# Optimization experiments

Hardware: AMD Instinct MI355X
Metric: run time of the kernel (lower is better)

## Reference

```python
import jax, jax.numpy as jnp
import numpy as np
from functools import partial

L, B, D_IN, D_MODEL, D_OUT, D_STATE = 2048, 8, 128, 256, 32, 16
D_INNER, DT_RANK, K_CONV = 2 * D_MODEL, D_MODEL // 16, 4
LOG2PI = float(np.log(2.0 * np.pi))


def setup_inputs() -> dict:
    key = jax.random.key(0)
    ks = jax.random.split(key, 16)
    sc = 0.02
    inp = {
        "s": jax.random.normal(ks[0], (L, B, D_IN), jnp.float32),
        "a": jax.random.normal(ks[1], (L, B, D_OUT), jnp.float32),
        # embedding linear
        "W_emb": jax.random.normal(ks[2], (D_IN, D_MODEL), jnp.float32) * sc,
        "b_emb": jnp.zeros((D_MODEL,), jnp.float32),
        # mamba block params
        "norm_w": jnp.ones((D_MODEL,), jnp.float32),
        "W_in": jax.random.normal(ks[3], (D_MODEL, 2 * D_INNER), jnp.float32) * sc,
        "conv_w": jax.random.normal(ks[4], (D_INNER, 1, K_CONV), jnp.float32) * sc,
        "conv_b": jnp.zeros((D_INNER,), jnp.float32),
        "W_x": jax.random.normal(ks[5], (D_INNER, DT_RANK + 2 * D_STATE), jnp.float32) * sc,
        "W_dt": jax.random.normal(ks[6], (DT_RANK, D_INNER), jnp.float32) * sc,
        "b_dt": jnp.full((D_INNER,), -2.0, jnp.float32),  # softplus(-2) ~ small init dt
        "A_log": jnp.broadcast_to(jnp.log(jnp.arange(1, D_STATE + 1, dtype=jnp.float32)), (D_INNER, D_STATE)).copy(),
        "D": jnp.ones((D_INNER,), jnp.float32),
        "W_out": jax.random.normal(ks[7], (D_INNER, D_MODEL), jnp.float32) * sc,
        # action head + log_std
        "W_head": jax.random.normal(ks[8], (D_MODEL, D_OUT), jnp.float32) * sc,
        "b_head": jnp.zeros((D_OUT,), jnp.float32),
        "log_std": jnp.zeros((D_OUT,), jnp.float32),
    }
    return inp


def _rmsnorm(x, w, eps=1e-5):
    return x * jax.lax.rsqrt(jnp.mean(x * x, axis=-1, keepdims=True) + eps) * w


def _silu(x):
    return x * jax.nn.sigmoid(x)


def _mamba_block(x, norm_w, W_in, conv_w, conv_b, W_x, W_dt, b_dt, A_log, D, W_out):
    # x: (B, L, d_model)
    resid = x
    xn = _rmsnorm(x, norm_w)
    xz = xn @ W_in                                  # (B, L, 2*d_inner)
    xp, z = jnp.split(xz, 2, axis=-1)
    # causal depthwise conv over time
    xc = jax.lax.conv_general_dilated(
        xp.transpose(0, 2, 1), conv_w, window_strides=(1,),
        padding=[(K_CONV - 1, 0)], feature_group_count=D_INNER,
        dimension_numbers=("NCH", "OIH", "NCH"))
    xp = _silu((xc + conv_b[None, :, None]).transpose(0, 2, 1))  # (B, L, d_inner)
    # input-dependent SSM params
    x_dbl = xp @ W_x                                # (B, L, dt_rank + 2*d_state)
    dt, Bm, Cm = jnp.split(x_dbl, [DT_RANK, DT_RANK + D_STATE], axis=-1)
    dt = jax.nn.softplus(dt @ W_dt + b_dt)          # (B, L, d_inner)
    A = -jnp.exp(A_log)                             # (d_inner, d_state)

    def step(h, t):
        dt_t, B_t, C_t, x_t = t                     # (B,d_i) (B,d_s) (B,d_s) (B,d_i)
        dA = jnp.exp(dt_t[..., None] * A)           # (B, d_inner, d_state)
        dBx = (dt_t * x_t)[..., None] * B_t[:, None, :]
        h = dA * h + dBx
        y = jnp.einsum("bds,bs->bd", h, C_t)
        return h, y

    h0 = jnp.zeros((x.shape[0], D_INNER, D_STATE), x.dtype)
    tm = lambda u: jnp.moveaxis(u, 1, 0)            # time-major
    _, ys = jax.lax.scan(step, h0, (tm(dt), tm(Bm), tm(Cm), tm(xp)))
    y = jnp.moveaxis(ys, 0, 1) + xp * D             # (B, L, d_inner)
    y = y * _silu(z)
    return y @ W_out + resid


def reference(s, a, W_emb, b_emb, norm_w, W_in, conv_w, conv_b, W_x, W_dt, b_dt,
              A_log, D, W_out, W_head, b_head, log_std):
    x = s @ W_emb + b_emb                           # (L, B, d_model)
    x = x.transpose(1, 0, 2)                        # (B, L, d_model)
    x = _mamba_block(x, norm_w, W_in, conv_w, conv_b, W_x, W_dt, b_dt, A_log, D, W_out)
    x = x.transpose(1, 0, 2)                        # (L, B, d_model)
    mu = x @ W_head + b_head                        # (L, B, d_out)
    # Normal(mu, exp(log_std)).log_prob(a).sum(-1)
    z = (a - mu) * jnp.exp(-log_std)
    logp = -0.5 * z * z - log_std - 0.5 * LOG2PI
    return logp.sum(axis=-1)                        # (L, B)
```

## Files before the change

### kernel.cpp

```cpp
#include <hip/hip_runtime.h>

typedef unsigned short u16;
typedef short bf16x8 __attribute__((ext_vector_type(8)));
typedef float floatx4 __attribute__((ext_vector_type(4)));

#define LSEQ 2048
#define BB 8
#define NTOK (LSEQ*BB)
#define DMODEL 256
#define DINNER 512
#define NSEG 128
#define SEG_N 32
#define SEG_L 64

__device__ __forceinline__ float siluf(float x){ return x / (1.f + __expf(-x)); }
__device__ __forceinline__ float b2f(u16 x){ return __uint_as_float(((unsigned)x) << 16); }
__device__ __forceinline__ u16 f2b(float f){
  unsigned u = __float_as_uint(f);
  unsigned r = (u + 0x7fffu + ((u >> 16) & 1u)) >> 16;
  return (u16)r;
}

__device__ __forceinline__ void gload16(const u16* g, u16* l) {
  __builtin_amdgcn_global_load_lds(
      (const __attribute__((address_space(1))) unsigned int*)g,
      (__attribute__((address_space(3))) unsigned int*)l, 16, 0, 0);
}

__device__ __forceinline__ void compute_dA(float dt, float As0, bool uni,
    const float* __restrict__ Alog, int c, float* dA)
{
  if (uni) {
    float p = __expf(dt*As0);
    float p2 = p*p, p4 = p2*p2, p8 = p4*p4;
    dA[0]=p;      dA[1]=p2;     dA[2]=p2*p;   dA[3]=p4;
    dA[4]=p4*p;   dA[5]=p4*p2;  dA[6]=p4*p2*p;dA[7]=p8;
    dA[8]=p8*p;   dA[9]=p8*p2;  dA[10]=p8*p2*p; dA[11]=p8*p4;
    dA[12]=p8*p4*p; dA[13]=p8*p4*p2; dA[14]=p8*p4*p2*p; dA[15]=p8*p8;
  } else {
    #pragma unroll
    for (int s = 0; s < 16; ++s) dA[s] = __expf(dt * (-__expf(Alog[c*16+s])));
  }
}

__global__ __launch_bounds__(256) void prep_k(
    const float* __restrict__ Wemb, const float* __restrict__ Win,
    const float* __restrict__ Wout, const float* __restrict__ Wx,
    const float* __restrict__ Wh,
    u16* __restrict__ WTe, u16* __restrict__ WTi, u16* __restrict__ WTo,
    u16* __restrict__ WxT, u16* __restrict__ WhT)
{
  __shared__ u16 T[64*66];
  int g = blockIdx.x, tid = threadIdx.x;
  if (g < 96) {
    const float* src; u16* dst; int n0, k0, srcld, dstld;
    if (g < 64) {
      int tn = g & 15, tk = g >> 4;
      n0 = tn*64; k0 = tk*64; src = Win; dst = WTi; srcld = 1024; dstld = 256;
    } else {
      int g2 = g - 64;
      int tn = g2 & 3, tk = g2 >> 2;
      n0 = tn*64; k0 = tk*64; src = Wout; dst = WTo; srcld = 256; dstld = 512;
    }
    int rr = tid >> 6, cc = tid & 63;
    #pragma unroll
    for (int p = 0; p < 16; ++p) {
      int kr = p*4 + rr;
      T[kr*66 + cc] = f2b(src[(size_t)(k0+kr)*srcld + n0 + cc]);
    }
    __syncthreads();
    #pragma unroll
    for (int p = 0; p < 16; ++p) {
      int nr = p*4 + rr;
      dst[(size_t)(n0+nr)*dstld + k0 + cc] = T[cc*66 + nr];
    }
  } else if (g < 224) {
    int idx = (g-96)*256 + tid; int n = idx >> 7, k = idx & 127;
    WTe[idx] = f2b(Wemb[(size_t)k*256 + n]);
  } else if (g < 320) {
    int idx = (g-224)*256 + tid; int n = idx >> 9, k = idx & 511;
    WxT[idx] = f2b(Wx[(size_t)k*48 + n]);
  } else {
    int idx = (g-320)*256 + tid; int j = idx >> 8, k = idx & 255;
    WhT[idx] = f2b(Wh[(size_t)k*32 + j]);
  }
}

__global__ __launch_bounds__(256) void embnorm_k(
    const float* __restrict__ s, const u16* __restrict__ WTe,
    const float* __restrict__ bemb, const float* __restrict__ nw,
    u16* __restrict__ Xb, u16* __restrict__ XNb)
{
  __shared__ u16 SH[64*264];
  __shared__ float ssq[64*4];
  __shared__ float rr[64];
  u16* As = SH;
  u16* Bs = SH + 64*40;
  const int tid = threadIdx.x;
  const int wave = tid >> 6, lane = tid & 63;
  const int quad = lane >> 4, l16 = lane & 15;
  const int m0 = blockIdx.x*64;
  const int wn = wave*64;
  const int srow = tid >> 2, sch = (tid & 3)*8;
  floatx4 acc[4][4];
  #pragma unroll
  for (int r = 0; r < 4; ++r)
    #pragma unroll
    for (int c = 0; c < 4; ++c) acc[r][c] = (floatx4){0.f,0.f,0.f,0.f};

  for (int k0 = 0; k0 < 128; k0 += 32) {
    {
      float4 v0 = *(const float4*)&s[(size_t)(m0+srow)*128 + k0 + sch];
      float4 v1 = *(const float4*)&s[(size_t)(m0+srow)*128 + k0 + sch + 4];
      __align__(16) u16 o[8];
      o[0]=f2b(v0.x); o[1]=f2b(v0.y); o[2]=f2b(v0.z); o[3]=f2b(v0.w);
      o[4]=f2b(v1.x); o[5]=f2b(v1.y); o[6]=f2b(v1.z); o[7]=f2b(v1.w);
      *(uint4*)&As[srow*40 + sch] = *(const uint4*)o;
    }
    #pragma unroll
    for (int p = 0; p < 4; ++p) {
      int row = srow + p*64;
      *(uint4*)&Bs[row*40 + sch] = *(const uint4*)&WTe[(size_t)row*128 + k0 + sch];
    }
    __syncthreads();
    bf16x8 af[4], bf[4];
    #pragma unroll
    for (int r = 0; r < 4; ++r) af[r] = *(const bf16x8*)&As[(r*16 + l16)*40 + quad*8];
    #pragma unroll
    for (int c = 0; c < 4; ++c) bf[c] = *(const bf16x8*)&Bs[(wn + c*16 + l16)*40 + quad*8];
    #pragma unroll
    for (int r = 0; r < 4; ++r)
      #pragma unroll
      for (int c = 0; c < 4; ++c)
        acc[r][c] = __builtin_amdgcn_mfma_f32_16x16x32_bf16(af[r], bf[c], acc[r][c], 0, 0, 0);
    __syncthreads();
  }
  u16* Xs = SH;
  #pragma unroll
  for (int c = 0; c < 4; ++c) {
    int n = wn + c*16 + l16;
    float bv = bemb[n];
    #pragma unroll
    for (int r = 0; r < 4; ++r)
      #pragma unroll
      for (int reg = 0; reg < 4; ++reg) {
        int ml = r*16 + quad*4 + reg;
        Xs[ml*264 + n] = f2b(acc[r][c][reg] + bv);
      }
  }
  __syncthreads();
  #pragma unroll
  for (int p = 0; p < 8; ++p) {
    int row = p*8 + (tid >> 5);
    int col = (tid & 31)*8;
    *(uint4*)&Xb[(size_t)(m0+row)*256 + col] = *(const uint4*)&Xs[row*264 + col];
  }
  const int tk = tid >> 2, q = tid & 3;
  float ss = 0.f;
  #pragma unroll
  for (int j = 0; j < 8; ++j) {
    uint4 v = *(const uint4*)&Xs[tk*264 + q*64 + j*8];
    const u16* u = (const u16*)&v;
    #pragma unroll
    for (int i = 0; i < 8; ++i) { float x = b2f(u[i]); ss += x*x; }
  }
  ssq[tk*4 + q] = ss;
  __syncthreads();
  if (q == 0)
    rr[tk] = rsqrtf((ssq[tk*4]+ssq[tk*4+1]+ssq[tk*4+2]+ssq[tk*4+3])*(1.f/DMODEL) + 1e-5f);
  __syncthreads();
  float r = rr[tk];
  #pragma unroll
  for (int j = 0; j < 8; ++j) {
    int idx = q*64 + j*8;
    uint4 v = *(const uint4*)&Xs[tk*264 + idx];
    const u16* u = (const u16*)&v;
    float4 w0 = *(const float4*)&nw[idx];
    float4 w1 = *(const float4*)&nw[idx+4];
    __align__(16) u16 o[8];
    o[0]=f2b(b2f(u[0])*r*w0.x); o[1]=f2b(b2f(u[1])*r*w0.y);
    o[2]=f2b(b2f(u[2])*r*w0.z); o[3]=f2b(b2f(u[3])*r*w0.w);
    o[4]=f2b(b2f(u[4])*r*w1.x); o[5]=f2b(b2f(u[5])*r*w1.y);
    o[6]=f2b(b2f(u[6])*r*w1.z); o[7]=f2b(b2f(u[7])*r*w1.w);
    *(uint4*)&XNb[(size_t)(m0+tk)*256 + idx] = *(const uint4*)o;
  }
}

template<int K>
__global__ __launch_bounds__(256) void gemm_mfma(
    const u16* __restrict__ Ab, const u16* __restrict__ WT,
    u16* __restrict__ Cv, int N)
{
  __shared__ __align__(16) u16 SH[17408];
  u16* As = SH;
  u16* Bs = SH + 128*64;
  const int tid = threadIdx.x;
  const int wave = tid >> 6, lane = tid & 63;
  const int quad = lane >> 4, l16 = lane & 15;
  const int bm0 = blockIdx.x*128, bn0 = blockIdx.y*128;
  const int wm = (wave & 1)*64, wn = (wave >> 1)*64;
  floatx4 acc[4][4];
  #pragma unroll
  for (int r = 0; r < 4; ++r)
    #pragma unroll
    for (int c = 0; c < 4; ++c) acc[r][c] = (floatx4){0.f,0.f,0.f,0.f};

  for (int k0 = 0; k0 < K; k0 += 64) {
    #pragma unroll
    for (int p = 0; p < 4; ++p) {
      int cid = (wave*4 + p)*64 + lane;
      int row = cid >> 3, sch = (cid & 7) ^ (row & 7);
      gload16(&Ab[(size_t)(bm0+row)*K + k0 + sch*8], As + (wave*4+p)*512);
      gload16(&WT[(size_t)(bn0+row)*K + k0 + sch*8], Bs + (wave*4+p)*512);
    }
    __syncthreads();
    #pragma unroll
    for (int ks = 0; ks < 2; ++ks) {
      bf16x8 af[4], bf[4];
      #pragma unroll
      for (int r = 0; r < 4; ++r) {
        int row = wm + r*16 + l16;
        int lch = (ks*4 + quad) ^ (row & 7);
        af[r] = *(const bf16x8*)&As[row*64 + lch*8];
      }
      #pragma unroll
      for (int c = 0; c < 4; ++c) {
        int row = wn + c*16 + l16;
        int lch = (ks*4 + quad) ^ (row & 7);
        bf[c] = *(const bf16x8*)&Bs[row*64 + lch*8];
      }
      #pragma unroll
      for (int r = 0; r < 4; ++r)
        #pragma unroll
        for (int c = 0; c < 4; ++c)
          acc[r][c] = __builtin_amdgcn_mfma_f32_16x16x32_bf16(af[r], bf[c], acc[r][c], 0, 0, 0);
    }
    __syncthreads();
  }
  u16* Cs = SH;
  #pragma unroll
  for (int c = 0; c < 4; ++c) {
    int nl = wn + c*16 + l16;
    #pragma unroll
    for (int r = 0; r < 4; ++r)
      #pragma unroll
      for (int reg = 0; reg < 4; ++reg) {
        int ml = wm + r*16 + quad*4 + reg;
        Cs[ml*136 + nl] = f2b(acc[r][c][reg]);
      }
  }
  __syncthreads();
  #pragma unroll
  for (int p = 0; p < 8; ++p) {
    int row = p*16 + (tid >> 4);
    int col = (tid & 15)*8;
    uint4 v = *(const uint4*)&Cs[row*136 + col];
    *(uint4*)&Cv[(size_t)(bm0+row)*N + bn0 + col] = v;
  }
}

__global__ __launch_bounds__(256) void xdblBC_k(const u16* __restrict__ XZb,
    const float* __restrict__ cw, const float* __restrict__ cb,
    const u16* __restrict__ WxT,
    float* __restrict__ BM, float* __restrict__ CM, float* __restrict__ DTR,
    u16* __restrict__ XPb)
{
  __shared__ u16 As[64*40];
  __shared__ u16 Ws[48*40];
  __shared__ float CWs[512*4];
  __shared__ float CBs[512];
  const int tid = threadIdx.x;
  const int wave = tid >> 6, lane = tid & 63;
  const int quad = lane >> 4, l16 = lane & 15;
  const int m0 = blockIdx.x*64;
  const int srow = tid >> 2, sch = (tid & 3)*8;
  const int n = m0 + srow;
  for (int e = tid; e < 2048; e += 256) CWs[e] = cw[e];
  for (int e = tid; e < 512;  e += 256) CBs[e] = cb[e];
  floatx4 acc[3];
  #pragma unroll
  for (int j = 0; j < 3; ++j) acc[j] = (floatx4){0.f,0.f,0.f,0.f};
  __syncthreads();
  const bf16x8 z8 = {0,0,0,0,0,0,0,0};
  for (int k0 = 0; k0 < DINNER; k0 += 32) {
    bf16x8 t3 = *(const bf16x8*)&XZb[(size_t)n*1024 + k0 + sch];
    bf16x8 t2 = z8, t1 = z8, t0v = z8;
    if (n >= 8)  t2  = *(const bf16x8*)&XZb[(size_t)(n-8)*1024  + k0 + sch];
    if (n >= 16) t1  = *(const bf16x8*)&XZb[(size_t)(n-16)*1024 + k0 + sch];
    if (n >= 24) t0v = *(const bf16x8*)&XZb[(size_t)(n-24)*1024 + k0 + sch];
    __align__(16) u16 outa[8];
    #pragma unroll
    for (int j = 0; j < 8; ++j) {
      int c = k0 + sch + j;
      float4 wv = *(const float4*)&CWs[c*4];
      float xc = CBs[c] + wv.x*b2f((u16)t0v[j]) + wv.y*b2f((u16)t1[j])
               + wv.z*b2f((u16)t2[j]) + wv.w*b2f((u16)t3[j]);
      outa[j] = f2b(siluf(xc));
    }
    *(uint4*)&As[srow*40 + sch] = *(const uint4*)outa;
    *(uint4*)&XPb[(size_t)n*DINNER + k0 + sch] = *(const uint4*)outa;
    if (tid < 192) {
      int wr = tid >> 2;
      *(uint4*)&Ws[wr*40 + sch] = *(const uint4*)&WxT[(size_t)wr*512 + k0 + sch];
    }
    __syncthreads();
    bf16x8 af = *(const bf16x8*)&As[(wave*16 + l16)*40 + quad*8];
    #pragma unroll
    for (int j = 0; j < 3; ++j) {
      bf16x8 bf = *(const bf16x8*)&Ws[(j*16 + l16)*40 + quad*8];
      acc[j] = __builtin_amdgcn_mfma_f32_16x16x32_bf16(af, bf, acc[j], 0, 0, 0);
    }
    __syncthreads();
  }
  const int tok0 = m0 + wave*16;
  #pragma unroll
  for (int reg = 0; reg < 4; ++reg) {
    size_t t = (size_t)(tok0 + quad*4 + reg);
    BM[t*16 + l16]  = acc[1][reg];
    CM[t*16 + l16]  = acc[2][reg];
    DTR[t*16 + l16] = acc[0][reg];
  }
}

__global__ __launch_bounds__(256) void scanA_k(const float* __restrict__ DTR,
    const u16* __restrict__ XPb, const float* __restrict__ BM,
    const float* __restrict__ Wdt, const float* __restrict__ bdt,
    const float* __restrict__ Alog, u16* __restrict__ HENDb,
    float* __restrict__ DTS, unsigned* __restrict__ DXb)
{
  __shared__ float ROWa[SEG_L*16];
  __shared__ float ROWb[SEG_L*16];
  const int tid = threadIdx.x;
  const int seg = blockIdx.x, b = blockIdx.y, half = blockIdx.z;
  const int c = half*256 + tid;
  const int t0 = seg*SEG_L;
  const size_t base = (size_t)t0*BB + b;
  for (int idx = tid; idx < SEG_L*16; idx += 256) {
    int t = idx >> 4, j = idx & 15;
    size_t off = (base + (size_t)t*BB)*16 + j;
    ROWa[idx] = BM[off];
    ROWb[idx] = DTR[off];
  }
  float As0 = -__expf(Alog[c*16]);
  bool uni = true;
  #pragma unroll
  for (int s = 1; s < 16; ++s) {
    float Av = -__expf(Alog[c*16+s]);
    uni = uni && (fabsf(Av - As0*(float)(s+1)) <= 1e-4f*(float)(s+1));
  }
  float wdt[16];
  #pragma unroll
  for (int r = 0; r < 16; ++r) wdt[r] = Wdt[r*DINNER + c];
  const float bd = bdt[c];
  float h[16];
  #pragma unroll
  for (int s = 0; s < 16; ++s) h[s] = 0.f;
  float dts = 0.f;
  const u16* xpp = XPb + base*DINNER + c;
  __syncthreads();
  float xp = b2f(xpp[0]);
  for (int t = 0; t < SEG_L; ++t) {
    float xpn = (t+1 < SEG_L) ? b2f(xpp[(size_t)(t+1)*BB*DINNER]) : 0.f;
    float dsum = bd;
    #pragma unroll
    for (int r = 0; r < 16; ++r) dsum = fmaf(ROWb[t*16+r], wdt[r], dsum);
    float dt = (dsum > 20.f) ? dsum : __logf(1.f + __expf(dsum));
    dts += dt;
    DXb[(((size_t)(t0+t)*BB + b)*DINNER + c)] = ((unsigned)f2b(xp) << 16) | f2b(dt);
    float dtx = dt * xp;
    float dA[16];
    compute_dA(dt, As0, uni, Alog, c, dA);
    float4 r0 = *(const float4*)&ROWa[t*16 + 0];
    float4 r1 = *(const float4*)&ROWa[t*16 + 4];
    float4 r2 = *(const float4*)&ROWa[t*16 + 8];
    float4 r3 = *(const float4*)&ROWa[t*16 + 12];
    h[0]  = fmaf(dA[0],  h[0],  dtx*r0.x);
    h[1]  = fmaf(dA[1],  h[1],  dtx*r0.y);
    h[2]  = fmaf(dA[2],  h[2],  dtx*r0.z);
    h[3]  = fmaf(dA[3],  h[3],  dtx*r0.w);
    h[4]  = fmaf(dA[4],  h[4],  dtx*r1.x);
    h[5]  = fmaf(dA[5],  h[5],  dtx*r1.y);
    h[6]  = fmaf(dA[6],  h[6],  dtx*r1.z);
    h[7]  = fmaf(dA[7],  h[7],  dtx*r1.w);
    h[8]  = fmaf(dA[8],  h[8],  dtx*r2.x);
    h[9]  = fmaf(dA[9],  h[9],  dtx*r2.y);
    h[10] = fmaf(dA[10], h[10], dtx*r2.z);
    h[11] = fmaf(dA[11], h[11], dtx*r2.w);
    h[12] = fmaf(dA[12], h[12], dtx*r3.x);
    h[13] = fmaf(dA[13], h[13], dtx*r3.y);
    h[14] = fmaf(dA[14], h[14], dtx*r3.z);
    h[15] = fmaf(dA[15], h[15], dtx*r3.w);
    xp = xpn;
  }
  u16* hp = &HENDb[(((size_t)seg*BB + b)*DINNER + c)*16];
  #pragma unroll
  for (int q = 0; q < 2; ++q) {
    ushort4 v0, v1;
    v0.x = f2b(h[q*8+0]); v0.y = f2b(h[q*8+1]); v0.z = f2b(h[q*8+2]); v0.w = f2b(h[q*8+3]);
    v1.x = f2b(h[q*8+4]); v1.y = f2b(h[q*8+5]); v1.z = f2b(h[q*8+6]); v1.w = f2b(h[q*8+7]);
    *(ushort4*)&hp[q*8]     = v0;
    *(ushort4*)&hp[q*8 + 4] = v1;
  }
  DTS[((size_t)seg*BB + b)*DINNER + c] = dts;
}

__global__ __launch_bounds__(256) void scanC_k(const unsigned* __restrict__ DXb,
    const u16* __restrict__ XZb, const float* __restrict__ BM, const float* __restrict__ CM,
    const float* __restrict__ Alog, const float* __restrict__ Dp,
    const u16* __restrict__ HENDb, const float* __restrict__ DTS,
    u16* __restrict__ YGb)
{
  __shared__ float ROWa[SEG_L*16];
  __shared__ float ROWc[SEG_L*16];
  const int tid = threadIdx.x;
  const int seg = (SEG_N - 1) - blockIdx.x;
  const int b = blockIdx.y, half = blockIdx.z;
  const int c = half*256 + tid;
  const int t0 = seg*SEG_L;
  const size_t base = (size_t)t0*BB + b;
  for (int idx = tid; idx < SEG_L*16; idx += 256) {
    int t = idx >> 4, j = idx & 15;
    size_t off = (base + (size_t)t*BB)*16 + j;
    ROWa[idx] = BM[off];
    ROWc[idx] = CM[off];
  }
  float As0 = -__expf(Alog[c*16]);
  bool uni = true;
  #pragma unroll
  for (int s = 1; s < 16; ++s) {
    float Av = -__expf(Alog[c*16+s]);
    uni = uni && (fabsf(Av - As0*(float)(s+1)) <= 1e-4f*(float)(s+1));
  }
  float h[16];
  #pragma unroll
  for (int s = 0; s < 16; ++s) h[s] = 0.f;
  if (seg > 0) {
    float ds = DTS[((size_t)0*BB + b)*DINNER + c];
    const u16* hp0 = &HENDb[(((size_t)0*BB + b)*DINNER + c)*16];
    ushort4 a0 = *(const ushort4*)&hp0[0];
    ushort4 a1 = *(const ushort4*)&hp0[4];
    ushort4 a2 = *(const ushort4*)&hp0[8];
    ushort4 a3 = *(const ushort4*)&hp0[12];
    for (int k = 0; k < seg; ++k) {
      float dsn = 0.f;
      ushort4 n0, n1, n2, n3;
      if (k+1 < seg) {
        dsn = DTS[((size_t)(k+1)*BB + b)*DINNER + c];
        const u16* hpn = &HENDb[(((size_t)(k+1)*BB + b)*DINNER + c)*16];
        n0 = *(const ushort4*)&hpn[0];
        n1 = *(const ushort4*)&hpn[4];
        n2 = *(const ushort4*)&hpn[8];
        n3 = *(const ushort4*)&hpn[12];
      }
      float dA[16];
      compute_dA(ds, As0, uni, Alog, c, dA);
      h[0]  = fmaf(h[0],  dA[0],  b2f(a0.x));
      h[1]  = fmaf(h[1],  dA[1],  b2f(a0.y));
      h[2]  = fmaf(h[2],  dA[2],  b2f(a0.z));
      h[3]  = fmaf(h[3],  dA[3],  b2f(a0.w));
      h[4]  = fmaf(h[4],  dA[4],  b2f(a1.x));
      h[5]  = fmaf(h[5],  dA[5],  b2f(a1.y));
      h[6]  = fmaf(h[6],  dA[6],  b2f(a1.z));
      h[7]  = fmaf(h[7],  dA[7],  b2f(a1.w));
      h[8]  = fmaf(h[8],  dA[8],  b2f(a2.x));
      h[9]  = fmaf(h[9],  dA[9],  b2f(a2.y));
      h[10] = fmaf(h[10], dA[10], b2f(a2.z));
      h[11] = fmaf(h[11], dA[11], b2f(a2.w));
      h[12] = fmaf(h[12], dA[12], b2f(a3.x));
      h[13] = fmaf(h[13], dA[13], b2f(a3.y));
      h[14] = fmaf(h[14], dA[14], b2f(a3.z));
      h[15] = fmaf(h[15], dA[15], b2f(a3.w));
      ds = dsn; a0 = n0; a1 = n1; a2 = n2; a3 = n3;
    }
  }
  const float Dv = Dp[c];
  const unsigned* dxp = DXb + base*DINNER + c;
  const u16* zp  = XZb + base*1024 + DINNER + c;
  u16*       ygp = YGb + base*DINNER + c;
  __syncthreads();
  unsigned dx = dxp[0];
  float zg = b2f(zp[0]);
  for (int t = 0; t < SEG_L; ++t) {
    unsigned dxn = 0; float zgn = 0.f;
    if (t+1 < SEG_L) {
      dxn = dxp[(size_t)(t+1)*BB*DINNER];
      zgn = b2f(zp[(size_t)(t+1)*BB*1024]);
    }
    float dt = __uint_as_float(dx << 16);
    float xp = __uint_as_float(dx & 0xffff0000u);
    float dtx = dt * xp;
    float dA[16];
    compute_dA(dt, As0, uni, Alog, c, dA);
    float4 ra0 = *(const float4*)&ROWa[t*16 + 0];
    float4 ra1 = *(const float4*)&ROWa[t*16 + 4];
    float4 ra2 = *(const float4*)&ROWa[t*16 + 8];
    float4 ra3 = *(const float4*)&ROWa[t*16 + 12];
    float4 rc0 = *(const float4*)&ROWc[t*16 + 0];
    float4 rc1 = *(const float4*)&ROWc[t*16 + 4];
    float4 rc2 = *(const float4*)&ROWc[t*16 + 8];
    float4 rc3 = *(const float4*)&ROWc[t*16 + 12];
    float y0 = 0.f, y1 = 0.f, y2 = 0.f, y3 = 0.f;
    h[0]  = fmaf(dA[0],  h[0],  dtx*ra0.x); y0 = fmaf(h[0],  rc0.x, y0);
    h[1]  = fmaf(dA[1],  h[1],  dtx*ra0.y); y1 = fmaf(h[1],  rc0.y, y1);
    h[2]  = fmaf(dA[2],  h[2],  dtx*ra0.z); y2 = fmaf(h[2],  rc0.z, y2);
    h[3]  = fmaf(dA[3],  h[3],  dtx*ra0.w); y3 = fmaf(h[3],  rc0.w, y3);
    h[4]  = fmaf(dA[4],  h[4],  dtx*ra1.x); y0 = fmaf(h[4],  rc1.x, y0);
    h[5]  = fmaf(dA[5],  h[5],  dtx*ra1.y); y1 = fmaf(h[5],  rc1.y, y1);
    h[6]  = fmaf(dA[6],  h[6],  dtx*ra1.z); y2 = fmaf(h[6],  rc1.z, y2);
    h[7]  = fmaf(dA[7],  h[7],  dtx*ra1.w); y3 = fmaf(h[7],  rc1.w, y3);
    h[8]  = fmaf(dA[8],  h[8],  dtx*ra2.x); y0 = fmaf(h[8],  rc2.x, y0);
    h[9]  = fmaf(dA[9],  h[9],  dtx*ra2.y); y1 = fmaf(h[9],  rc2.y, y1);
    h[10] = fmaf(dA[10], h[10], dtx*ra2.z); y2 = fmaf(h[10], rc2.z, y2);
    h[11] = fmaf(dA[11], h[11], dtx*ra2.w); y3 = fmaf(h[11], rc2.w, y3);
    h[12] = fmaf(dA[12], h[12], dtx*ra3.x); y0 = fmaf(h[12], rc3.x, y0);
    h[13] = fmaf(dA[13], h[13], dtx*ra3.y); y1 = fmaf(h[13], rc3.y, y1);
    h[14] = fmaf(dA[14], h[14], dtx*ra3.z); y2 = fmaf(h[14], rc3.z, y2);
    h[15] = fmaf(dA[15], h[15], dtx*ra3.w); y3 = fmaf(h[15], rc3.w, y3);
    float y = (y0+y1) + (y2+y3);
    ygp[(size_t)t*BB*DINNER] = f2b((y + xp*Dv) * siluf(zg));
    dx = dxn; zg = zgn;
  }
}

__global__ __launch_bounds__(256) void outhead_k(const u16* __restrict__ YGb,
    const u16* __restrict__ WTo, const u16* __restrict__ Xb,
    const u16* __restrict__ WhT, const float* __restrict__ bh,
    const float* __restrict__ lstd, const float* __restrict__ a,
    float* __restrict__ out)
{
  __shared__ u16 SH[(64+256)*72];
  u16* As = SH;
  u16* Bs = SH + 64*72;
  const int tid = threadIdx.x;
  const int wave = tid >> 6, lane = tid & 63;
  const int quad = lane >> 4, l16 = lane & 15;
  const int m0 = blockIdx.x*64;
  const int n0 = wave*64;
  const int srow = tid >> 3, sch = (tid & 7)*8;
  floatx4 acc[4][4];
  #pragma unroll
  for (int r = 0; r < 4; ++r)
    #pragma unroll
    for (int c = 0; c < 4; ++c) acc[r][c] = (floatx4){0.f,0.f,0.f,0.f};

  for (int k0 = 0; k0 < DINNER; k0 += 64) {
    #pragma unroll
    for (int p = 0; p < 2; ++p) {
      int row = srow + p*32;
      *(uint4*)&As[row*72 + sch] = *(const uint4*)&YGb[(size_t)(m0+row)*DINNER + k0 + sch];
    }
    #pragma unroll
    for (int p = 0; p < 8; ++p) {
      int row = srow + p*32;
      *(uint4*)&Bs[row*72 + sch] = *(const uint4*)&WTo[(size_t)row*DINNER + k0 + sch];
    }
    __syncthreads();
    #pragma unroll
    for (int ks = 0; ks < 2; ++ks) {
      bf16x8 af[4], bf[4];
      #pragma unroll
      for (int r = 0; r < 4; ++r)
        af[r] = *(const bf16x8*)&As[(r*16 + l16)*72 + ks*32 + quad*8];
      #pragma unroll
      for (int c = 0; c < 4; ++c)
        bf[c] = *(const bf16x8*)&Bs[(n0 + c*16 + l16)*72 + ks*32 + quad*8];
      #pragma unroll
      for (int r = 0; r < 4; ++r)
        #pragma unroll
        for (int c = 0; c < 4; ++c)
          acc[r][c] = __builtin_amdgcn_mfma_f32_16x16x32_bf16(af[r], bf[c], acc[r][c], 0, 0, 0);
    }
    __syncthreads();
  }
  u16* Xs = SH;
  #pragma unroll
  for (int p = 0; p < 8; ++p) {
    int row = p*8 + (tid >> 5);
    int col = (tid & 31)*8;
    *(uint4*)&Xs[row*264 + col] = *(const uint4*)&Xb[(size_t)(m0+row)*256 + col];
  }
  __syncthreads();
  #pragma unroll
  for (int c = 0; c < 4; ++c) {
    int n = n0 + c*16 + l16;
    #pragma unroll
    for (int r = 0; r < 4; ++r) {
      #pragma unroll
      for (int reg = 0; reg < 4; ++reg) {
        int ml = r*16 + quad*4 + reg;
        Xs[ml*264 + n] = f2b(acc[r][c][reg] + b2f(Xs[ml*264 + n]));
      }
    }
  }
  __syncthreads();
  floatx4 mu[2];
  mu[0] = (floatx4){0.f,0.f,0.f,0.f};
  mu[1] = (floatx4){0.f,0.f,0.f,0.f};
  #pragma unroll
  for (int k0 = 0; k0 < DMODEL; k0 += 32) {
    bf16x8 axf = *(const bf16x8*)&Xs[(wave*16 + l16)*264 + k0 + quad*8];
    #pragma unroll
    for (int nt = 0; nt < 2; ++nt) {
      bf16x8 bwf = *(const bf16x8*)(WhT + (size_t)(nt*16 + l16)*DMODEL + k0 + quad*8);
      mu[nt] = __builtin_amdgcn_mfma_f32_16x16x32_bf16(axf, bwf, mu[nt], 0, 0, 0);
    }
  }
  float ls0 = lstd[l16],      els0 = __expf(-ls0), bh0 = bh[l16];
  float ls1 = lstd[16 + l16], els1 = __expf(-ls1), bh1 = bh[16 + l16];
  #pragma unroll
  for (int reg = 0; reg < 4; ++reg) {
    int tok = m0 + wave*16 + quad*4 + reg;
    float m0v = mu[0][reg] + bh0;
    float m1v = mu[1][reg] + bh1;
    float z0 = (a[(size_t)tok*32 + l16]      - m0v) * els0;
    float z1 = (a[(size_t)tok*32 + 16 + l16] - m1v) * els1;
    float t = (-0.5f*z0*z0 - ls0) + (-0.5f*z1*z1 - ls1) - 2.f*0.91893853320467274f;
    t += __shfl_xor(t, 1);
    t += __shfl_xor(t, 2);
    t += __shfl_xor(t, 4);
    t += __shfl_xor(t, 8);
    if (l16 == 0) out[tok] = t;
  }
}

extern "C" void kernel_launch(void* const* d_in, const int* in_sizes, int n_in,
                              void* d_out, int out_size, void* d_ws, size_t ws_size,
                              hipStream_t stream)
{
  const float* s    = (const float*)d_in[0];
  const float* a    = (const float*)d_in[1];
  const float* Wemb = (const float*)d_in[2];
  const float* bemb = (const float*)d_in[3];
  const float* nw   = (const float*)d_in[4];
  const float* Win  = (const float*)d_in[5];
  const float* cw   = (const float*)d_in[6];
  const float* cb   = (const float*)d_in[7];
  const float* Wx   = (const float*)d_in[8];
  const float* Wdt  = (const float*)d_in[9];
  const float* bdt  = (const float*)d_in[10];
  const float* Alog = (const float*)d_in[11];
  const float* Dp   = (const float*)d_in[12];
  const float* Wout = (const float*)d_in[13];
  const float* Wh   = (const float*)d_in[14];
  const float* bh   = (const float*)d_in[15];
  const float* lstd = (const float*)d_in[16];

  u16*   Xb   = (u16*)d_ws;
  u16*   XZb  = Xb  + (size_t)NTOK*DMODEL;
  u16*   XNb  = XZb + (size_t)NTOK*1024;
  u16*   YGb  = XNb + (size_t)NTOK*DMODEL;
  u16*   WTe  = YGb + (size_t)NTOK*DINNER;
  u16*   WTi  = WTe + 256*128;
  u16*   WTo  = WTi + 1024*256;
  u16*   WxT  = WTo + 256*512;
  u16*   WhT  = WxT + 48*512;
  u16*   HENDb= WhT + 32*256;
  u16*   XPb  = HENDb + (size_t)NSEG*BB*DINNER*16;
  unsigned* DXb = (unsigned*)(XPb + (size_t)NTOK*DINNER);
  float* BM   = (float*)(DXb + (size_t)NTOK*DINNER);
  float* CM   = BM + (size_t)NTOK*16;
  float* DTR  = CM + (size_t)NTOK*16;
  float* DTS  = DTR + (size_t)NTOK*16;
  float* out  = (float*)d_out;

  prep_k        <<<352,         256, 0, stream>>>(Wemb, Win, Wout, Wx, Wh,
                                                  WTe, WTi, WTo, WxT, WhT);
  embnorm_k     <<<256,         256, 0, stream>>>(s, WTe, bemb, nw, Xb, XNb);
  gemm_mfma<256><<<dim3(128,8), 256, 0, stream>>>(XNb, WTi, XZb, 1024);
  xdblBC_k      <<<256,         256, 0, stream>>>(XZb, cw, cb, WxT, BM, CM, DTR, XPb);
  scanA_k       <<<dim3(SEG_N,BB,2), 256, 0, stream>>>(DTR, XPb, BM, Wdt, bdt,
                                                       Alog, HENDb, DTS, DXb);
  scanC_k       <<<dim3(SEG_N,BB,2), 256, 0, stream>>>(DXb, XZb, BM, CM,
                                                       Alog, Dp, HENDb, DTS, YGb);
  outhead_k     <<<256,         256, 0, stream>>>(YGb, WTo, Xb, WhT, bh, lstd, a, out);
}
```

Baseline: 241.2 us.

## Split scan state across lane pairs and halve segment length

Each channel's 16-element SSM state is now split across two half-waves of 8 states each. Partial dt and y sums are combined with a cross-lane shuffle, and the segment count doubles to 64 segments of length 32. Both scan kernels launch four times as many threads with fewer registers each, which raises parallelism and shortens the sequential time loop. In exchange there are extra shuffles, duplicated dt computation, half-idle lanes on stores, and a longer serial cross-segment combine in scanC.

After: 269.3 us. +11.7%, slower.

```diff
diff --git a/kernel.cpp b/kernel.cpp
--- a/kernel.cpp
+++ b/kernel.cpp
@@ -10,8 +10,8 @@
 #define DMODEL 256
 #define DINNER 512
 #define NSEG 128
-#define SEG_N 32
-#define SEG_L 64
+#define SEG_N 64
+#define SEG_L 32
 
 __device__ __forceinline__ float siluf(float x){ return x / (1.f + __expf(-x)); }
 __device__ __forceinline__ float b2f(u16 x){ return __uint_as_float(((unsigned)x) << 16); }
@@ -27,19 +27,19 @@
       (__attribute__((address_space(3))) unsigned int*)l, 16, 0, 0);
 }
 
-__device__ __forceinline__ void compute_dA(float dt, float As0, bool uni,
-    const float* __restrict__ Alog, int c, float* dA)
+__device__ __forceinline__ void compute_dA8(float dt, float As0, bool uni,
+    const float* __restrict__ Alog, int c, int so, float* dA)
 {
   if (uni) {
     float p = __expf(dt*As0);
-    float p2 = p*p, p4 = p2*p2, p8 = p4*p4;
-    dA[0]=p;      dA[1]=p2;     dA[2]=p2*p;   dA[3]=p4;
-    dA[4]=p4*p;   dA[5]=p4*p2;  dA[6]=p4*p2*p;dA[7]=p8;
-    dA[8]=p8*p;   dA[9]=p8*p2;  dA[10]=p8*p2*p; dA[11]=p8*p4;
-    dA[12]=p8*p4*p; dA[13]=p8*p4*p2; dA[14]=p8*p4*p2*p; dA[15]=p8*p8;
+    float p2 = p*p, p3 = p2*p, p4 = p2*p2;
+    float p5 = p4*p, p6 = p4*p2, p7 = p4*p3, p8 = p4*p4;
+    float f = so ? p8 : 1.f;
+    dA[0]=p*f;  dA[1]=p2*f; dA[2]=p3*f; dA[3]=p4*f;
+    dA[4]=p5*f; dA[5]=p6*f; dA[6]=p7*f; dA[7]=p8*f;
   } else {
     #pragma unroll
-    for (int s = 0; s < 16; ++s) dA[s] = __expf(dt * (-__expf(Alog[c*16+s])));
+    for (int j = 0; j < 8; ++j) dA[j] = __expf(dt * (-__expf(Alog[c*16+so+j])));
   }
 }
 
@@ -331,8 +331,10 @@
   __shared__ float ROWa[SEG_L*16];
   __shared__ float ROWb[SEG_L*16];
   const int tid = threadIdx.x;
-  const int seg = blockIdx.x, b = blockIdx.y, half = blockIdx.z;
-  const int c = half*256 + tid;
+  const int wave = tid >> 6, lane = tid & 63;
+  const int sgrp = lane >> 5, so = sgrp*8;
+  const int seg = blockIdx.x, b = blockIdx.y;
+  const int c = blockIdx.z*128 + wave*32 + (lane & 31);
   const int t0 = seg*SEG_L;
   const size_t base = (size_t)t0*BB + b;
   for (int idx = tid; idx < SEG_L*16; idx += 256) {
@@ -348,60 +350,51 @@
     float Av = -__expf(Alog[c*16+s]);
     uni = uni && (fabsf(Av - As0*(float)(s+1)) <= 1e-4f*(float)(s+1));
   }
-  float wdt[16];
-  #pragma unroll
-  for (int r = 0; r < 16; ++r) wdt[r] = Wdt[r*DINNER + c];
+  float wdt[8];
+  #pragma unroll
+  for (int r = 0; r < 8; ++r) wdt[r] = Wdt[(so + r)*DINNER + c];
   const float bd = bdt[c];
-  float h[16];
-  #pragma unroll
-  for (int s = 0; s < 16; ++s) h[s] = 0.f;
+  float h[8];
+  #pragma unroll
+  for (int j = 0; j < 8; ++j) h[j] = 0.f;
   float dts = 0.f;
   const u16* xpp = XPb + base*DINNER + c;
   __syncthreads();
   float xp = b2f(xpp[0]);
   for (int t = 0; t < SEG_L; ++t) {
     float xpn = (t+1 < SEG_L) ? b2f(xpp[(size_t)(t+1)*BB*DINNER]) : 0.f;
-    float dsum = bd;
-    #pragma unroll
-    for (int r = 0; r < 16; ++r) dsum = fmaf(ROWb[t*16+r], wdt[r], dsum);
+    float dpart = sgrp ? 0.f : bd;
+    #pragma unroll
+    for (int r = 0; r < 8; ++r) dpart = fmaf(ROWb[t*16 + so + r], wdt[r], dpart);
+    float dsum = dpart + __shfl_xor(dpart, 32);
     float dt = (dsum > 20.f) ? dsum : __logf(1.f + __expf(dsum));
     dts += dt;
-    DXb[(((size_t)(t0+t)*BB + b)*DINNER + c)] = ((unsigned)f2b(xp) << 16) | f2b(dt);
+    if (sgrp == 0)
+      DXb[(((size_t)(t0+t)*BB + b)*DINNER + c)] = ((unsigned)f2b(xp) << 16) | f2b(dt);
     float dtx = dt * xp;
-    float dA[16];
-    compute_dA(dt, As0, uni, Alog, c, dA);
-    float4 r0 = *(const float4*)&ROWa[t*16 + 0];
-    float4 r1 = *(const float4*)&ROWa[t*16 + 4];
-    float4 r2 = *(const float4*)&ROWa[t*16 + 8];
-    float4 r3 = *(const float4*)&ROWa[t*16 + 12];
-    h[0]  = fmaf(dA[0],  h[0],  dtx*r0.x);
-    h[1]  = fmaf(dA[1],  h[1],  dtx*r0.y);
-    h[2]  = fmaf(dA[2],  h[2],  dtx*r0.z);
-    h[3]  = fmaf(dA[3],  h[3],  dtx*r0.w);
-    h[4]  = fmaf(dA[4],  h[4],  dtx*r1.x);
-    h[5]  = fmaf(dA[5],  h[5],  dtx*r1.y);
-    h[6]  = fmaf(dA[6],  h[6],  dtx*r1.z);
-    h[7]  = fmaf(dA[7],  h[7],  dtx*r1.w);
-    h[8]  = fmaf(dA[8],  h[8],  dtx*r2.x);
-    h[9]  = fmaf(dA[9],  h[9],  dtx*r2.y);
-    h[10] = fmaf(dA[10], h[10], dtx*r2.z);
-    h[11] = fmaf(dA[11], h[11], dtx*r2.w);
-    h[12] = fmaf(dA[12], h[12], dtx*r3.x);
-    h[13] = fmaf(dA[13], h[13], dtx*r3.y);
-    h[14] = fmaf(dA[14], h[14], dtx*r3.z);
-    h[15] = fmaf(dA[15], h[15], dtx*r3.w);
+    float dA[8];
+    compute_dA8(dt, As0, uni, Alog, c, so, dA);
+    float4 r0 = *(const float4*)&ROWa[t*16 + so + 0];
+    float4 r1 = *(const float4*)&ROWa[t*16 + so + 4];
+    h[0] = fmaf(dA[0], h[0], dtx*r0.x);
+    h[1] = fmaf(dA[1], h[1], dtx*r0.y);
+    h[2] = fmaf(dA[2], h[2], dtx*r0.z);
+    h[3] = fmaf(dA[3], h[3], dtx*r0.w);
+    h[4] = fmaf(dA[4], h[4], dtx*r1.x);
+    h[5] = fmaf(dA[5], h[5], dtx*r1.y);
+    h[6] = fmaf(dA[6], h[6], dtx*r1.z);
+    h[7] = fmaf(dA[7], h[7], dtx*r1.w);
     xp = xpn;
   }
-  u16* hp = &HENDb[(((size_t)seg*BB + b)*DINNER + c)*16];
-  #pragma unroll
-  for (int q = 0; q < 2; ++q) {
-    ushort4 v0, v1;
-    v0.x = f2b(h[q*8+0]); v0.y = f2b(h[q*8+1]); v0.z = f2b(h[q*8+2]); v0.w = f2b(h[q*8+3]);
-    v1.x = f2b(h[q*8+4]); v1.y = f2b(h[q*8+5]); v1.z = f2b(h[q*8+6]); v1.w = f2b(h[q*8+7]);
-    *(ushort4*)&hp[q*8]     = v0;
-    *(ushort4*)&hp[q*8 + 4] = v1;
-  }
-  DTS[((size_t)seg*BB + b)*DINNER + c] = dts;
+  {
+    __align__(16) u16 o[8];
+    #pragma unroll
+    for (int j = 0; j < 8; ++j) o[j] = f2b(h[j]);
+    u16* hp = &HENDb[(((size_t)seg*BB + b)*DINNER + c)*16 + so];
+    *(uint4*)hp = *(const uint4*)o;
+  }
+  if (sgrp == 0)
+    DTS[((size_t)seg*BB + b)*DINNER + c] = dts;
 }
 
 __global__ __launch_bounds__(256) void scanC_k(const unsigned* __restrict__ DXb,
@@ -413,9 +406,11 @@
   __shared__ float ROWa[SEG_L*16];
   __shared__ float ROWc[SEG_L*16];
   const int tid = threadIdx.x;
+  const int wave = tid >> 6, lane = tid & 63;
+  const int sgrp = lane >> 5, so = sgrp*8;
   const int seg = (SEG_N - 1) - blockIdx.x;
-  const int b = blockIdx.y, half = blockIdx.z;
-  const int c = half*256 + tid;
+  const int b = blockIdx.y;
+  const int c = blockIdx.z*128 + wave*32 + (lane & 31);
   const int t0 = seg*SEG_L;
   const size_t base = (size_t)t0*BB + b;
   for (int idx = tid; idx < SEG_L*16; idx += 256) {
@@ -431,46 +426,31 @@
     float Av = -__expf(Alog[c*16+s]);
     uni = uni && (fabsf(Av - As0*(float)(s+1)) <= 1e-4f*(float)(s+1));
   }
-  float h[16];
-  #pragma unroll
-  for (int s = 0; s < 16; ++s) h[s] = 0.f;
+  float h[8];
+  #pragma unroll
+  for (int j = 0; j < 8; ++j) h[j] = 0.f;
   if (seg > 0) {
     float ds = DTS[((size_t)0*BB + b)*DINNER + c];
-    const u16* hp0 = &HENDb[(((size_t)0*BB + b)*DINNER + c)*16];
-    ushort4 a0 = *(const ushort4*)&hp0[0];
-    ushort4 a1 = *(const ushort4*)&hp0[4];
-    ushort4 a2 = *(const ushort4*)&hp0[8];
-    ushort4 a3 = *(const ushort4*)&hp0[12];
+    uint4 hv = *(const uint4*)&HENDb[(((size_t)0*BB + b)*DINNER + c)*16 + so];
     for (int k = 0; k < seg; ++k) {
       float dsn = 0.f;
-      ushort4 n0, n1, n2, n3;
+      uint4 hn = hv;
       if (k+1 < seg) {
         dsn = DTS[((size_t)(k+1)*BB + b)*DINNER + c];
-        const u16* hpn = &HENDb[(((size_t)(k+1)*BB + b)*DINNER + c)*16];
-        n0 = *(const ushort4*)&hpn[0];
-        n1 = *(const ushort4*)&hpn[4];
-        n2 = *(const ushort4*)&hpn[8];
-        n3 = *(const ushort4*)&hpn[12];
+        hn = *(const uint4*)&HENDb[(((size_t)(k+1)*BB + b)*DINNER + c)*16 + so];
       }
-      float dA[16];
-      compute_dA(ds, As0, uni, Alog, c, dA);
-      h[0]  = fmaf(h[0],  dA[0],  b2f(a0.x));
-      h[1]  = fmaf(h[1],  dA[1],  b2f(a0.y));
-      h[2]  = fmaf(h[2],  dA[2],  b2f(a0.z));
-      h[3]  = fmaf(h[3],  dA[3],  b2f(a0.w));
-      h[4]  = fmaf(h[4],  dA[4],  b2f(a1.x));
-      h[5]  = fmaf(h[5],  dA[5],  b2f(a1.y));
-      h[6]  = fmaf(h[6],  dA[6],  b2f(a1.z));
-      h[7]  = fmaf(h[7],  dA[7],  b2f(a1.w));
-      h[8]  = fmaf(h[8],  dA[8],  b2f(a2.x));
-      h[9]  = fmaf(h[9],  dA[9],  b2f(a2.y));
-      h[10] = fmaf(h[10], dA[10], b2f(a2.z));
-      h[11] = fmaf(h[11], dA[11], b2f(a2.w));
-      h[12] = fmaf(h[12], dA[12], b2f(a3.x));
-      h[13] = fmaf(h[13], dA[13], b2f(a3.y));
-      h[14] = fmaf(h[14], dA[14], b2f(a3.z));
-      h[15] = fmaf(h[15], dA[15], b2f(a3.w));
-      ds = dsn; a0 = n0; a1 = n1; a2 = n2; a3 = n3;
+      const u16* he = (const u16*)&hv;
+      float dA[8];
+      compute_dA8(ds, As0, uni, Alog, c, so, dA);
+      h[0] = fmaf(h[0], dA[0], b2f(he[0]));
+      h[1] = fmaf(h[1], dA[1], b2f(he[1]));
+      h[2] = fmaf(h[2], dA[2], b2f(he[2]));
+      h[3] = fmaf(h[3], dA[3], b2f(he[3]));
+      h[4] = fmaf(h[4], dA[4], b2f(he[4]));
+      h[5] = fmaf(h[5], dA[5], b2f(he[5]));
+      h[6] = fmaf(h[6], dA[6], b2f(he[6]));
+      h[7] = fmaf(h[7], dA[7], b2f(he[7]));
+      ds = dsn; hv = hn;
     }
   }
   const float Dv = Dp[c];
@@ -489,35 +469,25 @@
     float dt = __uint_as_float(dx << 16);
     float xp = __uint_as_float(dx & 0xffff0000u);
     float dtx = dt * xp;
-    float dA[16];
-    compute_dA(dt, As0, uni, Alog, c, dA);
-    float4 ra0 = *(const float4*)&ROWa[t*16 + 0];
-    float4 ra1 = *(const float4*)&ROWa[t*16 + 4];
-    float4 ra2 = *(const float4*)&ROWa[t*16 + 8];
-    float4 ra3 = *(const float4*)&ROWa[t*16 + 12];
-    float4 rc0 = *(const float4*)&ROWc[t*16 + 0];
-    float4 rc1 = *(const float4*)&ROWc[t*16 + 4];
-    float4 rc2 = *(const float4*)&ROWc[t*16 + 8];
-    float4 rc3 = *(const float4*)&ROWc[t*16 + 12];
+    float dA[8];
+    compute_dA8(dt, As0, uni, Alog, c, so, dA);
+    float4 ra0 = *(const float4*)&ROWa[t*16 + so + 0];
+    float4 ra1 = *(const float4*)&ROWa[t*16 + so + 4];
+    float4 rc0 = *(const float4*)&ROWc[t*16 + so + 0];
+    float4 rc1 = *(const float4*)&ROWc[t*16 + so + 4];
     float y0 = 0.f, y1 = 0.f, y2 = 0.f, y3 = 0.f;
-    h[0]  = fmaf(dA[0],  h[0],  dtx*ra0.x); y0 = fmaf(h[0],  rc0.x, y0);
-    h[1]  = fmaf(dA[1],  h[1],  dtx*ra0.y); y1 = fmaf(h[1],  rc0.y, y1);
-    h[2]  = fmaf(dA[2],  h[2],  dtx*ra0.z); y2 = fmaf(h[2],  rc0.z, y2);
-    h[3]  = fmaf(dA[3],  h[3],  dtx*ra0.w); y3 = fmaf(h[3],  rc0.w, y3);
-    h[4]  = fmaf(dA[4],  h[4],  dtx*ra1.x); y0 = fmaf(h[4],  rc1.x, y0);
-    h[5]  = fmaf(dA[5],  h[5],  dtx*ra1.y); y1 = fmaf(h[5],  rc1.y, y1);
-    h[6]  = fmaf(dA[6],  h[6],  dtx*ra1.z); y2 = fmaf(h[6],  rc1.z, y2);
-    h[7]  = fmaf(dA[7],  h[7],  dtx*ra1.w); y3 = fmaf(h[7],  rc1.w, y3);
-    h[8]  = fmaf(dA[8],  h[8],  dtx*ra2.x); y0 = fmaf(h[8],  rc2.x, y0);
-    h[9]  = fmaf(dA[9],  h[9],  dtx*ra2.y); y1 = fmaf(h[9],  rc2.y, y1);
-    h[10] = fmaf(dA[10], h[10], dtx*ra2.z); y2 = fmaf(h[10], rc2.z, y2);
-    h[11] = fmaf(dA[11], h[11], dtx*ra2.w); y3 = fmaf(h[11], rc2.w, y3);
-    h[12] = fmaf(dA[12], h[12], dtx*ra3.x); y0 = fmaf(h[12], rc3.x, y0);
-    h[13] = fmaf(dA[13], h[13], dtx*ra3.y); y1 = fmaf(h[13], rc3.y, y1);
-    h[14] = fmaf(dA[14], h[14], dtx*ra3.z); y2 = fmaf(h[14], rc3.z, y2);
-    h[15] = fmaf(dA[15], h[15], dtx*ra3.w); y3 = fmaf(h[15], rc3.w, y3);
-    float y = (y0+y1) + (y2+y3);
-    ygp[(size_t)t*BB*DINNER] = f2b((y + xp*Dv) * siluf(zg));
+    h[0] = fmaf(dA[0], h[0], dtx*ra0.x); y0 = fmaf(h[0], rc0.x, y0);
+    h[1] = fmaf(dA[1], h[1], dtx*ra0.y); y1 = fmaf(h[1], rc0.y, y1);
+    h[2] = fmaf(dA[2], h[2], dtx*ra0.z); y2 = fmaf(h[2], rc0.z, y2);
+    h[3] = fmaf(dA[3], h[3], dtx*ra0.w); y3 = fmaf(h[3], rc0.w, y3);
+    h[4] = fmaf(dA[4], h[4], dtx*ra1.x); y0 = fmaf(h[4], rc1.x, y0);
+    h[5] = fmaf(dA[5], h[5], dtx*ra1.y); y1 = fmaf(h[5], rc1.y, y1);
+    h[6] = fmaf(dA[6], h[6], dtx*ra1.z); y2 = fmaf(h[6], rc1.z, y2);
+    h[7] = fmaf(dA[7], h[7], dtx*ra1.w); y3 = fmaf(h[7], rc1.w, y3);
+    float yp = (y0+y1) + (y2+y3);
+    float y = yp + __shfl_xor(yp, 32);
+    if (sgrp == 0)
+      ygp[(size_t)t*BB*DINNER] = f2b((y + xp*Dv) * siluf(zg));
     dx = dxn; zg = zgn;
   }
 }
@@ -668,9 +638,9 @@
   embnorm_k     <<<256,         256, 0, stream>>>(s, WTe, bemb, nw, Xb, XNb);
   gemm_mfma<256><<<dim3(128,8), 256, 0, stream>>>(XNb, WTi, XZb, 1024);
   xdblBC_k      <<<256,         256, 0, stream>>>(XZb, cw, cb, WxT, BM, CM, DTR, XPb);
-  scanA_k       <<<dim3(SEG_N,BB,2), 256, 0, stream>>>(DTR, XPb, BM, Wdt, bdt,
+  scanA_k       <<<dim3(SEG_N,BB,4), 256, 0, stream>>>(DTR, XPb, BM, Wdt, bdt,
                                                        Alog, HENDb, DTS, DXb);
-  scanC_k       <<<dim3(SEG_N,BB,2), 256, 0, stream>>>(DXb, XZb, BM, CM,
+  scanC_k       <<<dim3(SEG_N,BB,4), 256, 0, stream>>>(DXb, XZb, BM, CM,
                                                        Alog, Dp, HENDb, DTS, YGb);
   outhead_k     <<<256,         256, 0, stream>>>(YGb, WTo, Xb, WhT, bh, lstd, a, out);
 }
```
